# Kernel tuning notes

Measured on AMD Instinct MI355X. Metric: run time of the kernel, lower is better.

The kernel has to match this reference:

```python
import jax, jax.numpy as jnp
import numpy as np

B, L, S, H, E, D = 2, 2048, 2048, 16, 64, 64

def setup_inputs() -> dict:
    key = jax.random.key(0)
    kq, kk, kv = jax.random.split(key, 3)
    queries = jax.random.normal(kq, (B, L, H, E), dtype=jnp.float32)
    keys = jax.random.normal(kk, (B, S, H, E), dtype=jnp.float32)
    values = jax.random.normal(kv, (B, S, H, D), dtype=jnp.float32)
    # TriangularCausalMask: True above the diagonal (masked positions)
    causal = jnp.triu(jnp.ones((L, S), dtype=bool), k=1)
    attn_mask = jnp.broadcast_to(causal[None, None], (B, 1, L, S))
    z = jnp.zeros((1,), dtype=jnp.float32)
    return {"queries": queries, "keys": keys, "values": values,
            "query_omegas": z, "query_thetas": z, "key_omegas": z,
            "key_thetas": z, "attn_mask": attn_mask}

def reference(queries, keys, values, query_omegas, query_thetas,
              key_omegas, key_thetas, attn_mask):
    # omegas/thetas are unused in FullAttention.forward (kept for signature parity)
    scale = 1.0 / jnp.sqrt(jnp.float32(E))
    scores = jnp.einsum('blhe,bshe->bhls', queries, keys)  # [B,H,L,S]
    scores = jnp.where(attn_mask, -jnp.inf, scores)
    A = jax.nn.softmax(scale * scores, axis=-1)  # dropout p=0 (eval)
    V = jnp.einsum('bhls,bshd->blhd', A, values)
    return V
```

## Files before the change

kernel.cpp:

```cpp
#include <hip/hip_runtime.h>
#include <hip/hip_bf16.h>
#include <math.h>

typedef __attribute__((ext_vector_type(8))) short bf16x8;
typedef __attribute__((ext_vector_type(16))) float f32x16;

#define B_ 2
#define L_ 2048
#define S_ 2048
#define H_ 16
#define E_ 64
#define D_ 64

#if __has_builtin(__builtin_amdgcn_exp2f)
#define EXP2(x) __builtin_amdgcn_exp2f(x)
#else
#define EXP2(x) exp2f(x)
#endif

__device__ __forceinline__ unsigned pkbf(float a, float b) {
  __hip_bfloat162 h = __float22bfloat162_rn(float2{a, b});
  return *(unsigned*)&h;
}

__device__ __forceinline__ int crow(int r, int hi5) {
  return (r & 3) + ((r >> 2) << 3) + (hi5 << 2);
}

__global__ __launch_bounds__(256, 2)
void fa_fwd5(const float* __restrict__ Qp, const float* __restrict__ Kp,
             const float* __restrict__ Vp, float* __restrict__ Op) {
  __shared__ uint4 sbuf[2][1024];

  const int tid  = threadIdx.x;
  const int lane = tid & 63;
  const int w    = tid >> 6;
  const int l31  = lane & 31;
  const int hi5  = lane >> 5;

  const int Bx   = blockIdx.x;
  const int r_   = (Bx >> 5) & 7;
  const int bh   = Bx & 31;
  const int b    = bh >> 4, h = bh & 15;
  const int qidx = (Bx >> 8) ? (7 - r_) : (8 + r_);
  const int q0   = qidx << 7;
  const int qw   = q0 + w * 32;
  const int nt   = 2 * qidx + 2;

  const float cs = 0.125f * 1.44269504088896f;

  const int krow = tid >> 2, ksg = tid & 3;
  const int vd   = tid & 63, kg  = tid >> 6;
  const int kswz = (krow & 7) << 4;
  const int vswz = (vd & 7) << 4;

  bf16x8 qf[4];
  {
    const int qg = qw + l31;
    const float* gq = Qp + ((size_t)(b * L_ + qg) * H_ + h) * E_ + hi5 * 8;
    #pragma unroll
    for (int ec = 0; ec < 4; ++ec) {
      float4 a = *(const float4*)(gq + ec * 16);
      float4 c = *(const float4*)(gq + ec * 16 + 4);
      uint4 u;
      u.x = pkbf(a.x * cs, a.y * cs);
      u.y = pkbf(a.z * cs, a.w * cs);
      u.z = pkbf(c.x * cs, c.y * cs);
      u.w = pkbf(c.z * cs, c.w * cs);
      qf[ec] = *(bf16x8*)&u;
    }
  }

  f32x16 acc[2];
  #pragma unroll
  for (int dt = 0; dt < 2; ++dt)
    #pragma unroll
    for (int rr = 0; rr < 16; ++rr) acc[dt][rr] = 0.f;

  float mrun = -INFINITY;
  float lsum = 0.f;

  {
    char* lk = (char*)&sbuf[0][0];
    char* lv = lk + 8192;
    const float* gk = Kp + ((size_t)(b * S_ + krow) * H_ + h) * E_ + ksg * 8;
    #pragma unroll
    for (int j = 0; j < 2; ++j) {
      float4 a = *(const float4*)(gk + j * 32);
      float4 c = *(const float4*)(gk + j * 32 + 4);
      uint4 u;
      u.x = pkbf(a.x, a.y); u.y = pkbf(a.z, a.w);
      u.z = pkbf(c.x, c.y); u.w = pkbf(c.z, c.w);
      *(uint4*)(lk + ((krow * 128 + ksg * 16 + j * 64) ^ kswz)) = u;
    }
    #pragma unroll
    for (int j = 0; j < 2; ++j) {
      const float* gv = Vp + ((size_t)(b * S_ + kg * 16 + j * 8) * H_ + h) * D_ + vd;
      float v0 = gv[(size_t)0 * (H_ * D_)];
      float v1 = gv[(size_t)1 * (H_ * D_)];
      float v2 = gv[(size_t)2 * (H_ * D_)];
      float v3 = gv[(size_t)3 * (H_ * D_)];
      float v4 = gv[(size_t)4 * (H_ * D_)];
      float v5 = gv[(size_t)5 * (H_ * D_)];
      float v6 = gv[(size_t)6 * (H_ * D_)];
      float v7 = gv[(size_t)7 * (H_ * D_)];
      uint4 u;
      u.x = pkbf(v0, v1); u.y = pkbf(v2, v3);
      u.z = pkbf(v4, v5); u.w = pkbf(v6, v7);
      *(uint4*)(lv + ((vd * 128 + kg * 32 + j * 16) ^ vswz)) = u;
    }
  }
  __syncthreads();

  int cur = 0;
  for (int t = 0; t < nt; ++t, cur ^= 1) {
    const int kv0 = t * 64;
    const bool have_next = (t + 1) < nt;

    float4 Ka[2], Kc[2];
    float Vv[16];
    if (have_next) {
      const int kvn = kv0 + 64;
      const float* gk = Kp + ((size_t)(b * S_ + kvn + krow) * H_ + h) * E_ + ksg * 8;
      Ka[0] = *(const float4*)(gk);
      Kc[0] = *(const float4*)(gk + 4);
      Ka[1] = *(const float4*)(gk + 32);
      Kc[1] = *(const float4*)(gk + 36);
      #pragma unroll
      for (int j = 0; j < 2; ++j) {
        const float* gv = Vp + ((size_t)(b * S_ + kvn + kg * 16 + j * 8) * H_ + h) * D_ + vd;
        #pragma unroll
        for (int k2 = 0; k2 < 8; ++k2)
          Vv[j * 8 + k2] = gv[(size_t)k2 * (H_ * D_)];
      }
    }

    if (kv0 <= qw + 31) {
      char* lk = (char*)&sbuf[cur][0];
      char* lv = lk + 8192;
      const bool needmask = (kv0 + 63) > qw;

      f32x16 st[2];
      #pragma unroll
      for (int c = 0; c < 2; ++c)
        #pragma unroll
        for (int rr = 0; rr < 16; ++rr) st[c][rr] = 0.f;
      #pragma unroll
      for (int c = 0; c < 2; ++c) {
        const int row = c * 32 + l31;
        const int sw = (row & 7) << 4;
        #pragma unroll
        for (int ec = 0; ec < 4; ++ec) {
          bf16x8 kf = *(bf16x8*)(lk + ((row * 128 + ec * 32 + hi5 * 16) ^ sw));
          st[c] = __builtin_amdgcn_mfma_f32_32x32x16_bf16(kf, qf[ec], st[c], 0, 0, 0);
        }
      }

      if (needmask) {
        const int qg = qw + l31;
        #pragma unroll
        for (int c = 0; c < 2; ++c)
          #pragma unroll
          for (int rr = 0; rr < 16; ++rr)
            if (kv0 + c * 32 + crow(rr, hi5) > qg) st[c][rr] = -1e30f;
      }

      float pm = st[0][0];
      #pragma unroll
      for (int c = 0; c < 2; ++c)
        #pragma unroll
        for (int rr = 0; rr < 16; ++rr) pm = fmaxf(pm, st[c][rr]);
      pm = fmaxf(pm, __shfl_xor(pm, 32));

      if (__any(pm > mrun + 8.f)) {
        const float mn = fmaxf(mrun, pm);
        const float f = EXP2(mrun - mn);
        mrun = mn;
        lsum *= f;
        #pragma unroll
        for (int rr = 0; rr < 16; ++rr) {
          const float fr = __shfl(f, crow(rr, hi5));
          acc[0][rr] *= fr;
          acc[1][rr] *= fr;
        }
      }
      {
        float ps = 0.f;
        #pragma unroll
        for (int c = 0; c < 2; ++c)
          #pragma unroll
          for (int rr = 0; rr < 16; ++rr) {
            st[c][rr] = EXP2(st[c][rr] - mrun);
            ps += st[c][rr];
          }
        ps += __shfl_xor(ps, 32);
        lsum += ps;
      }

      uint4 pa[4];
      #pragma unroll
      for (int c = 0; c < 2; ++c) {
        unsigned Dw[8];
        #pragma unroll
        for (int j = 0; j < 8; ++j)
          Dw[j] = pkbf(st[c][2 * j], st[c][2 * j + 1]);
        unsigned y0 = __shfl_xor((int)(hi5 ? Dw[0] : Dw[2]), 32);
        unsigned y1 = __shfl_xor((int)(hi5 ? Dw[1] : Dw[3]), 32);
        unsigned y2 = __shfl_xor((int)(hi5 ? Dw[4] : Dw[6]), 32);
        unsigned y3 = __shfl_xor((int)(hi5 ? Dw[5] : Dw[7]), 32);
        uint4 p0, p1;
        if (hi5) {
          p0 = uint4{y0, y1, Dw[2], Dw[3]};
          p1 = uint4{y2, y3, Dw[6], Dw[7]};
        } else {
          p0 = uint4{Dw[0], Dw[1], y0, y1};
          p1 = uint4{Dw[4], Dw[5], y2, y3};
        }
        pa[2 * c]     = p0;
        pa[2 * c + 1] = p1;
      }

      #pragma unroll
      for (int s = 0; s < 4; ++s) {
        #pragma unroll
        for (int dt = 0; dt < 2; ++dt) {
          const int row = dt * 32 + l31;
          bf16x8 vf = *(bf16x8*)(lv + ((row * 128 + s * 32 + hi5 * 16) ^ ((row & 7) << 4)));
          acc[dt] = __builtin_amdgcn_mfma_f32_32x32x16_bf16(*(bf16x8*)&pa[s], vf, acc[dt], 0, 0, 0);
        }
      }
    }

    if (have_next) {
      char* lk = (char*)&sbuf[cur ^ 1][0];
      char* lv = lk + 8192;
      #pragma unroll
      for (int j = 0; j < 2; ++j) {
        uint4 u;
        u.x = pkbf(Ka[j].x, Ka[j].y); u.y = pkbf(Ka[j].z, Ka[j].w);
        u.z = pkbf(Kc[j].x, Kc[j].y); u.w = pkbf(Kc[j].z, Kc[j].w);
        *(uint4*)(lk + ((krow * 128 + ksg * 16 + j * 64) ^ kswz)) = u;
      }
      #pragma unroll
      for (int j = 0; j < 2; ++j) {
        uint4 u;
        u.x = pkbf(Vv[j * 8 + 0], Vv[j * 8 + 1]);
        u.y = pkbf(Vv[j * 8 + 2], Vv[j * 8 + 3]);
        u.z = pkbf(Vv[j * 8 + 4], Vv[j * 8 + 5]);
        u.w = pkbf(Vv[j * 8 + 6], Vv[j * 8 + 7]);
        *(uint4*)(lv + ((vd * 128 + kg * 32 + j * 16) ^ vswz)) = u;
      }
    }
    __syncthreads();
  }

  {
    const float inv = 1.f / lsum;
    #pragma unroll
    for (int rr = 0; rr < 16; ++rr) {
      const float wr = __shfl(inv, crow(rr, hi5));
      const int qg = qw + crow(rr, hi5);
      float* go = Op + ((size_t)(b * L_ + qg) * H_ + h) * D_ + l31;
      go[0]  = acc[0][rr] * wr;
      go[32] = acc[1][rr] * wr;
    }
  }
}

extern "C" void kernel_launch(void* const* d_in, const int* in_sizes, int n_in,
                              void* d_out, int out_size, void* d_ws, size_t ws_size,
                              hipStream_t stream) {
  (void)in_sizes; (void)n_in; (void)d_ws; (void)ws_size; (void)out_size;
  const float* Q = (const float*)d_in[0];
  const float* K = (const float*)d_in[1];
  const float* V = (const float*)d_in[2];
  float* O = (float*)d_out;
  fa_fwd5<<<dim3(512), dim3(256), 0, stream>>>(Q, K, V, O);
}
```

Before: 55.61 us.

## Split attention into K/V pre-convert, split-KV main pass, and merge kernels

Measured after the change: 63.83 us. 14.8% more time.

```diff
diff --git a/kernel.cpp b/kernel.cpp
--- a/kernel.cpp
+++ b/kernel.cpp
@@ -11,48 +11,92 @@
 #define H_ 16
 #define E_ 64
 #define D_ 64
-
-#if __has_builtin(__builtin_amdgcn_exp2f)
-#define EXP2(x) __builtin_amdgcn_exp2f(x)
-#else
 #define EXP2(x) exp2f(x)
-#endif
+
+#define KOFF 0ull
+#define VOFF (8ull << 20)
+#define POFF (16ull << 20)
+#define SLOT_BYTES 18432ull
+#define NSLOTS 1120ull
+#define WS_NEED (POFF + NSLOTS * SLOT_BYTES)
+
+#define GLL(gp, lp) __builtin_amdgcn_global_load_lds( \
+    (const __attribute__((address_space(1))) unsigned int*)(gp), \
+    (__attribute__((address_space(3))) unsigned int*)(lp), 16, 0, 0)
 
 __device__ __forceinline__ unsigned pkbf(float a, float b) {
-  __hip_bfloat162 h = __float22bfloat162_rn(float2{a, b});
-  return *(unsigned*)&h;
-}
-
+  __hip_bfloat162 hh = __float22bfloat162_rn(float2{a, b});
+  return *(unsigned*)&hh;
+}
+__device__ __forceinline__ float bf2f(unsigned us) {
+  return __uint_as_float(us << 16);
+}
 __device__ __forceinline__ int crow(int r, int hi5) {
   return (r & 3) + ((r >> 2) << 3) + (hi5 << 2);
 }
-
-__global__ __launch_bounds__(256, 2)
-void fa_fwd5(const float* __restrict__ Qp, const float* __restrict__ Kp,
-             const float* __restrict__ Vp, float* __restrict__ Op) {
+__device__ __forceinline__ int nchunks(int q) { return (q >= 10) ? 3 : ((q >= 3) ? 2 : 1); }
+__device__ __forceinline__ int slotoff(int q, int c) {
+  return (q < 3) ? q : (q < 10) ? 3 + (q - 3) * 2 + c : 17 + (q - 10) * 3 + c;
+}
+
+__global__ __launch_bounds__(256)
+void fa_pre(const float* __restrict__ Kp, const float* __restrict__ Vp,
+            char* __restrict__ ws) {
+  const int Bx = blockIdx.x;
+  const int bh = Bx & 31, t = Bx >> 5;
+  const int b = bh >> 4, h = bh & 15;
+  const int kv0 = t * 64;
+  const int tid = threadIdx.x;
+  char* dk = ws + KOFF + ((size_t)(bh * 32 + t)) * 8192;
+  char* dv = ws + VOFF + ((size_t)(bh * 32 + t)) * 8192;
+  const int krow = tid >> 2, ksg = tid & 3;
+  const int kswz = (krow & 7) << 4;
+  const float* gk = Kp + ((size_t)(b * S_ + kv0 + krow) * H_ + h) * E_ + ksg * 16;
+  float4 a0 = ((const float4*)gk)[0], a1 = ((const float4*)gk)[1];
+  float4 a2 = ((const float4*)gk)[2], a3 = ((const float4*)gk)[3];
+  uint4 u0{pkbf(a0.x, a0.y), pkbf(a0.z, a0.w), pkbf(a1.x, a1.y), pkbf(a1.z, a1.w)};
+  uint4 u1{pkbf(a2.x, a2.y), pkbf(a2.z, a2.w), pkbf(a3.x, a3.y), pkbf(a3.z, a3.w)};
+  *(uint4*)(dk + ((krow * 128 + ksg * 32) ^ kswz)) = u0;
+  *(uint4*)(dk + ((krow * 128 + ksg * 32 + 16) ^ kswz)) = u1;
+  const int vd = tid & 63, kg = tid >> 6;
+  const int vswz = (vd & 7) << 4;
+  const float* gv = Vp + ((size_t)(b * S_ + kv0 + kg * 16) * H_ + h) * D_ + vd;
+  float v[16];
+  #pragma unroll
+  for (int k = 0; k < 16; ++k) v[k] = gv[(size_t)k * (H_ * D_)];
+  uint4 w0{pkbf(v[0], v[1]), pkbf(v[2], v[3]), pkbf(v[4], v[5]), pkbf(v[6], v[7])};
+  uint4 w1{pkbf(v[8], v[9]), pkbf(v[10], v[11]), pkbf(v[12], v[13]), pkbf(v[14], v[15])};
+  *(uint4*)(dv + ((vd * 128 + kg * 32) ^ vswz)) = w0;
+  *(uint4*)(dv + ((vd * 128 + kg * 32 + 16) ^ vswz)) = w1;
+}
+
+__global__ __launch_bounds__(256, 3)
+void fa_main(const float* __restrict__ Qp, char* __restrict__ ws) {
   __shared__ uint4 sbuf[2][1024];
 
   const int tid  = threadIdx.x;
   const int lane = tid & 63;
-  const int w    = tid >> 6;
+  const int sub  = tid >> 6;
   const int l31  = lane & 31;
   const int hi5  = lane >> 5;
 
-  const int Bx   = blockIdx.x;
-  const int r_   = (Bx >> 5) & 7;
-  const int bh   = Bx & 31;
-  const int b    = bh >> 4, h = bh & 15;
-  const int qidx = (Bx >> 8) ? (7 - r_) : (8 + r_);
-  const int q0   = qidx << 7;
-  const int qw   = q0 + w * 32;
-  const int nt   = 2 * qidx + 2;
+  const int Bx  = blockIdx.x;
+  const int xcd = Bx & 7, i_ = Bx >> 3;
+  const int bh  = xcd * 4 + (i_ & 3);
+  const int j   = i_ >> 2;
+  int q, c;
+  if (j < 18)      { q = 15 - j / 3;       c = j % 3; }
+  else if (j < 32) { q = 9 - (j - 18) / 2; c = (j - 18) & 1; }
+  else             { q = 34 - j;           c = 0; }
+  const int b = bh >> 4, h = bh & 15;
+  const int tot = 2 * q + 2, nc = nchunks(q);
+  const int base = tot / nc, rem = tot - base * nc;
+  const int R  = base + (c < rem ? 1 : 0);
+  const int t0 = c * base + (c < rem ? c : rem);
+  const int q0 = q << 7;
+  const int qw = q0 + sub * 32;
 
   const float cs = 0.125f * 1.44269504088896f;
-
-  const int krow = tid >> 2, ksg = tid & 3;
-  const int vd   = tid & 63, kg  = tid >> 6;
-  const int kswz = (krow & 7) << 4;
-  const int vswz = (vd & 7) << 4;
 
   bf16x8 qf[4];
   {
@@ -61,12 +105,12 @@
     #pragma unroll
     for (int ec = 0; ec < 4; ++ec) {
       float4 a = *(const float4*)(gq + ec * 16);
-      float4 c = *(const float4*)(gq + ec * 16 + 4);
+      float4 cc = *(const float4*)(gq + ec * 16 + 4);
       uint4 u;
       u.x = pkbf(a.x * cs, a.y * cs);
       u.y = pkbf(a.z * cs, a.w * cs);
-      u.z = pkbf(c.x * cs, c.y * cs);
-      u.w = pkbf(c.z * cs, c.w * cs);
+      u.z = pkbf(cc.x * cs, cc.y * cs);
+      u.w = pkbf(cc.z * cs, cc.w * cs);
       qf[ec] = *(bf16x8*)&u;
     }
   }
@@ -76,65 +120,27 @@
   for (int dt = 0; dt < 2; ++dt)
     #pragma unroll
     for (int rr = 0; rr < 16; ++rr) acc[dt][rr] = 0.f;
-
-  float mrun = -INFINITY;
-  float lsum = 0.f;
-
-  {
-    char* lk = (char*)&sbuf[0][0];
-    char* lv = lk + 8192;
-    const float* gk = Kp + ((size_t)(b * S_ + krow) * H_ + h) * E_ + ksg * 8;
-    #pragma unroll
-    for (int j = 0; j < 2; ++j) {
-      float4 a = *(const float4*)(gk + j * 32);
-      float4 c = *(const float4*)(gk + j * 32 + 4);
-      uint4 u;
-      u.x = pkbf(a.x, a.y); u.y = pkbf(a.z, a.w);
-      u.z = pkbf(c.x, c.y); u.w = pkbf(c.z, c.w);
-      *(uint4*)(lk + ((krow * 128 + ksg * 16 + j * 64) ^ kswz)) = u;
-    }
-    #pragma unroll
-    for (int j = 0; j < 2; ++j) {
-      const float* gv = Vp + ((size_t)(b * S_ + kg * 16 + j * 8) * H_ + h) * D_ + vd;
-      float v0 = gv[(size_t)0 * (H_ * D_)];
-      float v1 = gv[(size_t)1 * (H_ * D_)];
-      float v2 = gv[(size_t)2 * (H_ * D_)];
-      float v3 = gv[(size_t)3 * (H_ * D_)];
-      float v4 = gv[(size_t)4 * (H_ * D_)];
-      float v5 = gv[(size_t)5 * (H_ * D_)];
-      float v6 = gv[(size_t)6 * (H_ * D_)];
-      float v7 = gv[(size_t)7 * (H_ * D_)];
-      uint4 u;
-      u.x = pkbf(v0, v1); u.y = pkbf(v2, v3);
-      u.z = pkbf(v4, v5); u.w = pkbf(v6, v7);
-      *(uint4*)(lv + ((vd * 128 + kg * 32 + j * 16) ^ vswz)) = u;
-    }
-  }
+  float mrun = -INFINITY, lsum = 0.f;
+
+  const char* gK = ws + KOFF + ((size_t)bh * 32) * 8192;
+  const char* gV = ws + VOFF + ((size_t)bh * 32) * 8192;
+
+#define STAGE(buf_, t_) do {                                        \
+    const char* sk = gK + (size_t)(t_) * 8192 + tid * 16;           \
+    const char* sv = gV + (size_t)(t_) * 8192 + tid * 16;           \
+    char* lb = (char*)&sbuf[(buf_)][0] + tid * 16;                  \
+    GLL(sk, lb); GLL(sk + 4096, lb + 4096);                         \
+    GLL(sv, lb + 8192); GLL(sv + 4096, lb + 12288);                 \
+  } while (0)
+
+  STAGE(0, t0);
   __syncthreads();
 
   int cur = 0;
-  for (int t = 0; t < nt; ++t, cur ^= 1) {
+  for (int t = t0; t < t0 + R; ++t, cur ^= 1) {
+    if (t + 1 < t0 + R) STAGE(cur ^ 1, t + 1);
+
     const int kv0 = t * 64;
-    const bool have_next = (t + 1) < nt;
-
-    float4 Ka[2], Kc[2];
-    float Vv[16];
-    if (have_next) {
-      const int kvn = kv0 + 64;
-      const float* gk = Kp + ((size_t)(b * S_ + kvn + krow) * H_ + h) * E_ + ksg * 8;
-      Ka[0] = *(const float4*)(gk);
-      Kc[0] = *(const float4*)(gk + 4);
-      Ka[1] = *(const float4*)(gk + 32);
-      Kc[1] = *(const float4*)(gk + 36);
-      #pragma unroll
-      for (int j = 0; j < 2; ++j) {
-        const float* gv = Vp + ((size_t)(b * S_ + kvn + kg * 16 + j * 8) * H_ + h) * D_ + vd;
-        #pragma unroll
-        for (int k2 = 0; k2 < 8; ++k2)
-          Vv[j * 8 + k2] = gv[(size_t)k2 * (H_ * D_)];
-      }
-    }
-
     if (kv0 <= qw + 31) {
       char* lk = (char*)&sbuf[cur][0];
       char* lv = lk + 8192;
@@ -142,34 +148,36 @@
 
       f32x16 st[2];
       #pragma unroll
-      for (int c = 0; c < 2; ++c)
-        #pragma unroll
-        for (int rr = 0; rr < 16; ++rr) st[c][rr] = 0.f;
-      #pragma unroll
-      for (int c = 0; c < 2; ++c) {
-        const int row = c * 32 + l31;
+      for (int c2 = 0; c2 < 2; ++c2)
+        #pragma unroll
+        for (int rr = 0; rr < 16; ++rr) st[c2][rr] = 0.f;
+      __builtin_amdgcn_s_setprio(1);
+      #pragma unroll
+      for (int c2 = 0; c2 < 2; ++c2) {
+        const int row = c2 * 32 + l31;
         const int sw = (row & 7) << 4;
         #pragma unroll
         for (int ec = 0; ec < 4; ++ec) {
           bf16x8 kf = *(bf16x8*)(lk + ((row * 128 + ec * 32 + hi5 * 16) ^ sw));
-          st[c] = __builtin_amdgcn_mfma_f32_32x32x16_bf16(kf, qf[ec], st[c], 0, 0, 0);
+          st[c2] = __builtin_amdgcn_mfma_f32_32x32x16_bf16(kf, qf[ec], st[c2], 0, 0, 0);
         }
       }
+      __builtin_amdgcn_s_setprio(0);
 
       if (needmask) {
         const int qg = qw + l31;
         #pragma unroll
-        for (int c = 0; c < 2; ++c)
+        for (int c2 = 0; c2 < 2; ++c2)
           #pragma unroll
           for (int rr = 0; rr < 16; ++rr)
-            if (kv0 + c * 32 + crow(rr, hi5) > qg) st[c][rr] = -1e30f;
+            if (kv0 + c2 * 32 + crow(rr, hi5) > qg) st[c2][rr] = -1e30f;
       }
 
       float pm = st[0][0];
       #pragma unroll
-      for (int c = 0; c < 2; ++c)
-        #pragma unroll
-        for (int rr = 0; rr < 16; ++rr) pm = fmaxf(pm, st[c][rr]);
+      for (int c2 = 0; c2 < 2; ++c2)
+        #pragma unroll
+        for (int rr = 0; rr < 16; ++rr) pm = fmaxf(pm, st[c2][rr]);
       pm = fmaxf(pm, __shfl_xor(pm, 32));
 
       if (__any(pm > mrun + 8.f)) {
@@ -187,11 +195,11 @@
       {
         float ps = 0.f;
         #pragma unroll
-        for (int c = 0; c < 2; ++c)
+        for (int c2 = 0; c2 < 2; ++c2)
           #pragma unroll
           for (int rr = 0; rr < 16; ++rr) {
-            st[c][rr] = EXP2(st[c][rr] - mrun);
-            ps += st[c][rr];
+            st[c2][rr] = EXP2(st[c2][rr] - mrun);
+            ps += st[c2][rr];
           }
         ps += __shfl_xor(ps, 32);
         lsum += ps;
@@ -199,11 +207,11 @@
 
       uint4 pa[4];
       #pragma unroll
-      for (int c = 0; c < 2; ++c) {
+      for (int c2 = 0; c2 < 2; ++c2) {
         unsigned Dw[8];
         #pragma unroll
-        for (int j = 0; j < 8; ++j)
-          Dw[j] = pkbf(st[c][2 * j], st[c][2 * j + 1]);
+        for (int jj = 0; jj < 8; ++jj)
+          Dw[jj] = pkbf(st[c2][2 * jj], st[c2][2 * jj + 1]);
         unsigned y0 = __shfl_xor((int)(hi5 ? Dw[0] : Dw[2]), 32);
         unsigned y1 = __shfl_xor((int)(hi5 ? Dw[1] : Dw[3]), 32);
         unsigned y2 = __shfl_xor((int)(hi5 ? Dw[4] : Dw[6]), 32);
@@ -216,10 +224,11 @@
           p0 = uint4{Dw[0], Dw[1], y0, y1};
           p1 = uint4{Dw[4], Dw[5], y2, y3};
         }
-        pa[2 * c]     = p0;
-        pa[2 * c + 1] = p1;
-      }
-
+        pa[2 * c2]     = p0;
+        pa[2 * c2 + 1] = p1;
+      }
+
+      __builtin_amdgcn_s_setprio(1);
       #pragma unroll
       for (int s = 0; s < 4; ++s) {
         #pragma unroll
@@ -229,51 +238,100 @@
           acc[dt] = __builtin_amdgcn_mfma_f32_32x32x16_bf16(*(bf16x8*)&pa[s], vf, acc[dt], 0, 0, 0);
         }
       }
-    }
-
-    if (have_next) {
-      char* lk = (char*)&sbuf[cur ^ 1][0];
-      char* lv = lk + 8192;
-      #pragma unroll
-      for (int j = 0; j < 2; ++j) {
-        uint4 u;
-        u.x = pkbf(Ka[j].x, Ka[j].y); u.y = pkbf(Ka[j].z, Ka[j].w);
-        u.z = pkbf(Kc[j].x, Kc[j].y); u.w = pkbf(Kc[j].z, Kc[j].w);
-        *(uint4*)(lk + ((krow * 128 + ksg * 16 + j * 64) ^ kswz)) = u;
-      }
-      #pragma unroll
-      for (int j = 0; j < 2; ++j) {
-        uint4 u;
-        u.x = pkbf(Vv[j * 8 + 0], Vv[j * 8 + 1]);
-        u.y = pkbf(Vv[j * 8 + 2], Vv[j * 8 + 3]);
-        u.z = pkbf(Vv[j * 8 + 4], Vv[j * 8 + 5]);
-        u.w = pkbf(Vv[j * 8 + 6], Vv[j * 8 + 7]);
-        *(uint4*)(lv + ((vd * 128 + kg * 32 + j * 16) ^ vswz)) = u;
-      }
+      __builtin_amdgcn_s_setprio(0);
     }
     __syncthreads();
   }
 
+  char* slot = ws + POFF + ((size_t)(bh * 35 + slotoff(q, c))) * SLOT_BYTES;
+  uint4* pw = (uint4*)(slot + (size_t)(sub * 64 + lane) * 64);
+  #pragma unroll
+  for (int dt = 0; dt < 2; ++dt) {
+    uint4 A{pkbf(acc[dt][0], acc[dt][1]),  pkbf(acc[dt][2], acc[dt][3]),
+            pkbf(acc[dt][4], acc[dt][5]),  pkbf(acc[dt][6], acc[dt][7])};
+    uint4 Bq{pkbf(acc[dt][8], acc[dt][9]),  pkbf(acc[dt][10], acc[dt][11]),
+             pkbf(acc[dt][12], acc[dt][13]), pkbf(acc[dt][14], acc[dt][15])};
+    pw[dt * 2]     = A;
+    pw[dt * 2 + 1] = Bq;
+  }
+  ((float2*)(slot + 16384))[sub * 64 + lane] = float2{mrun, lsum};
+#undef STAGE
+}
+
+__device__ __forceinline__ void unpk(uint4 a, uint4 b, float* o) {
+  const unsigned* pa = (const unsigned*)&a;
+  const unsigned* pb = (const unsigned*)&b;
+  #pragma unroll
+  for (int i = 0; i < 4; ++i) {
+    o[2 * i]     = bf2f(pa[i] & 0xffffu);
+    o[2 * i + 1] = bf2f(pa[i] >> 16);
+    o[8 + 2 * i]     = bf2f(pb[i] & 0xffffu);
+    o[8 + 2 * i + 1] = bf2f(pb[i] >> 16);
+  }
+}
+
+__global__ __launch_bounds__(256)
+void fa_merge(float* __restrict__ Op, const char* __restrict__ ws) {
+  const int Bx = blockIdx.x;
+  const int bh = Bx >> 4, q = Bx & 15;
+  const int b = bh >> 4, h = bh & 15;
+  const int tid = threadIdx.x, lane = tid & 63, sub = tid >> 6;
+  const int l31 = lane & 31, hi5 = lane >> 5;
+  const int nc = nchunks(q);
+  const char* sbase = ws + POFF;
+
+  float A0[16], A1[16], M, Lw;
   {
-    const float inv = 1.f / lsum;
+    const char* s0 = sbase + ((size_t)(bh * 35 + slotoff(q, 0))) * SLOT_BYTES;
+    const uint4* pr = (const uint4*)(s0 + (size_t)(sub * 64 + lane) * 64);
+    unpk(pr[0], pr[1], A0);
+    unpk(pr[2], pr[3], A1);
+    float2 ml = ((const float2*)(s0 + 16384))[sub * 64 + lane];
+    M = ml.x; Lw = ml.y;
+  }
+  for (int ci = 1; ci < nc; ++ci) {
+    const char* si = sbase + ((size_t)(bh * 35 + slotoff(q, ci))) * SLOT_BYTES;
+    const uint4* pr = (const uint4*)(si + (size_t)(sub * 64 + lane) * 64);
+    float a0[16], a1[16];
+    unpk(pr[0], pr[1], a0);
+    unpk(pr[2], pr[3], a1);
+    float2 ml = ((const float2*)(si + 16384))[sub * 64 + lane];
+    const float mm = fmaxf(M, ml.x);
+    const float fA = EXP2(M - mm);
+    const float fI = EXP2(ml.x - mm);
+    Lw = Lw * fA + ml.y * fI;
+    M = mm;
     #pragma unroll
     for (int rr = 0; rr < 16; ++rr) {
-      const float wr = __shfl(inv, crow(rr, hi5));
-      const int qg = qw + crow(rr, hi5);
-      float* go = Op + ((size_t)(b * L_ + qg) * H_ + h) * D_ + l31;
-      go[0]  = acc[0][rr] * wr;
-      go[32] = acc[1][rr] * wr;
+      const int cr = crow(rr, hi5);
+      const float fAb = __shfl(fA, cr);
+      const float fIb = __shfl(fI, cr);
+      A0[rr] = A0[rr] * fAb + a0[rr] * fIb;
+      A1[rr] = A1[rr] * fAb + a1[rr] * fIb;
     }
+  }
+  const float inv = 1.f / Lw;
+  #pragma unroll
+  for (int rr = 0; rr < 16; ++rr) {
+    const int cr = crow(rr, hi5);
+    const float wv = __shfl(inv, cr);
+    const int qg = (q << 7) + sub * 32 + cr;
+    float* go = Op + ((size_t)(b * L_ + qg) * H_ + h) * D_ + l31;
+    go[0]  = A0[rr] * wv;
+    go[32] = A1[rr] * wv;
   }
 }
 
 extern "C" void kernel_launch(void* const* d_in, const int* in_sizes, int n_in,
                               void* d_out, int out_size, void* d_ws, size_t ws_size,
                               hipStream_t stream) {
-  (void)in_sizes; (void)n_in; (void)d_ws; (void)ws_size; (void)out_size;
+  (void)in_sizes; (void)n_in; (void)out_size; (void)ws_size;
   const float* Q = (const float*)d_in[0];
   const float* K = (const float*)d_in[1];
   const float* V = (const float*)d_in[2];
   float* O = (float*)d_out;
-  fa_fwd5<<<dim3(512), dim3(256), 0, stream>>>(Q, K, V, O);
-}
+  char* ws = (char*)d_ws;
+  fa_pre<<<dim3(1024), dim3(256), 0, stream>>>(K, V, ws);
+  fa_main<<<dim3(1120), dim3(256), 0, stream>>>(Q, ws);
+  fa_merge<<<dim3(512), dim3(256), 0, stream>>>(O, ws);
+}
```
